# Performance work log

Measured on AMD Instinct MI355X. Metric: run time of the kernel, lower is better.

Reference implementation:

```python
import jax, jax.numpy as jnp
import numpy as np

T0, T1, LENGTH = 844, 1264, 8137


def setup_inputs() -> dict:
    key = jax.random.key(0)
    kq, = jax.random.split(key, 1)
    q = jax.random.normal(kq, (4, 8, LENGTH), dtype=jnp.float32)
    alpha0 = jnp.array(0.4886, dtype=jnp.float32)
    alpha1 = jnp.array(0.3893, dtype=jnp.float32)
    return {"q": q, "alpha0": alpha0, "alpha1": alpha1}


def reference(q, alpha0, alpha1):
    # A = I + alpha0 * superdiag(offset T0) + alpha1 * superdiag(offset T1)
    A = (jnp.eye(LENGTH, dtype=q.dtype)
         + alpha0 * jnp.eye(LENGTH, k=T0, dtype=q.dtype)
         + alpha1 * jnp.eye(LENGTH, k=T1, dtype=q.dtype))
    A_inv = jnp.linalg.inv(A)          # [L, L] dense inverse
    x = q @ A_inv                       # [B, C, L]
    loss = jnp.sum(x[0, 0, -T1:] ** 2)  # scalar
    return loss
```

## Files before the change

kernel.cpp:

```cpp
#include <hip/hip_runtime.h>


#define LENGTH 8137
#define T0 844
#define T1 1264

__global__ __launch_bounds__(256) void iir_loss_kernel(const float* __restrict__ q,
                                                       const float* __restrict__ alpha0,
                                                       const float* __restrict__ alpha1,
                                                       float* __restrict__ out) {
    __shared__ float x[LENGTH];
    __shared__ float partial[4];

    const float a0 = alpha0[0];
    const float a1 = alpha1[0];
    const int tid = threadIdx.x;

    const int nchunks = (LENGTH + T0 - 1) / T0;
    for (int c = 0; c < nchunks; ++c) {
        const int start = c * T0;
        const int end = (start + T0 < LENGTH) ? (start + T0) : LENGTH;
        for (int j = start + tid; j < end; j += 256) {
            float v = q[j];
            if (j >= T0) v -= a0 * x[j - T0];
            if (j >= T1) v -= a1 * x[j - T1];
            x[j] = v;
        }
        __syncthreads();
    }

    float s = 0.f;
    for (int j = (LENGTH - T1) + tid; j < LENGTH; j += 256) {
        s += x[j] * x[j];
    }
    for (int off = 32; off > 0; off >>= 1)
        s += __shfl_down(s, off, 64);
    const int wave = tid >> 6;
    if ((tid & 63) == 0) partial[wave] = s;
    __syncthreads();
    if (tid == 0) {
        float tot = partial[0] + partial[1] + partial[2] + partial[3];
        out[0] = tot;
    }
}

extern "C" void kernel_launch(void* const* d_in, const int* in_sizes, int n_in,
                              void* d_out, int out_size, void* d_ws, size_t ws_size,
                              hipStream_t stream) {
    const float* q      = (const float*)d_in[0];
    const float* alpha0 = (const float*)d_in[1];
    const float* alpha1 = (const float*)d_in[2];
    float* out = (float*)d_out;

    iir_loss_kernel<<<1, 256, 0, stream>>>(q, alpha0, alpha1, out);
}
```

Baseline: 68.20 us.

## Replace sequential IIR recurrence with closed-form binomial impulse-response expansion

Measured after the change: 59.81 us. -12.3%, faster.

```diff
diff --git a/kernel.cpp b/kernel.cpp
--- a/kernel.cpp
+++ b/kernel.cpp
@@ -4,44 +4,69 @@
 #define LENGTH 8137
 #define T0 844
 #define T1 1264
+#define JSTART (LENGTH - T1)
+#define MMAX 9
+#define NMAX 6
 
 __global__ __launch_bounds__(256) void iir_loss_kernel(const float* __restrict__ q,
-                                                       const float* __restrict__ alpha0,
-                                                       const float* __restrict__ alpha1,
+                                                       const float* __restrict__ a0p,
+                                                       const float* __restrict__ a1p,
                                                        float* __restrict__ out) {
-    __shared__ float x[LENGTH];
+    __shared__ float xq[LENGTH];
+    __shared__ float coef[NMAX + 1][MMAX + 1];
     __shared__ float partial[4];
 
-    const float a0 = alpha0[0];
-    const float a1 = alpha1[0];
     const int tid = threadIdx.x;
+    const float a0 = a0p[0];
+    const float a1 = a1p[0];
 
-    const int nchunks = (LENGTH + T0 - 1) / T0;
-    for (int c = 0; c < nchunks; ++c) {
-        const int start = c * T0;
-        const int end = (start + T0 < LENGTH) ? (start + T0) : LENGTH;
-        for (int j = start + tid; j < end; j += 256) {
-            float v = q[j];
-            if (j >= T0) v -= a0 * x[j - T0];
-            if (j >= T1) v -= a1 * x[j - T1];
-            x[j] = v;
+    const float4* q4 = reinterpret_cast<const float4*>(q);
+    for (int i = tid; i < LENGTH / 4; i += 256) {
+        float4 v = q4[i];
+        xq[4 * i + 0] = v.x;
+        xq[4 * i + 1] = v.y;
+        xq[4 * i + 2] = v.z;
+        xq[4 * i + 3] = v.w;
+    }
+    if (tid == 0) {
+        xq[LENGTH - 1] = q[LENGTH - 1];
+        coef[0][0] = 1.f;
+        for (int m = 1; m <= MMAX; ++m) coef[0][m] = -a0 * coef[0][m - 1];
+        for (int n = 1; n <= NMAX; ++n) {
+            coef[n][0] = -a1 * coef[n - 1][0];
+            for (int m = 1; m <= MMAX; ++m)
+                coef[n][m] = -a0 * coef[n][m - 1] - a1 * coef[n - 1][m];
         }
-        __syncthreads();
+    }
+    __syncthreads();
+
+    float v0 = 0.f, v1 = 0.f, v2 = 0.f, v3 = 0.f, v4 = 0.f;
+    const int j0 = JSTART + tid;
+    const bool has4 = (tid < (T1 - 4 * 256));
+
+    for (int n = 0; n <= NMAX; ++n) {
+        const int sn = T1 * n;
+        for (int m = 0; m <= MMAX; ++m) {
+            const int shift = sn + T0 * m;
+            if (shift >= LENGTH) break;
+            const float c = coef[n][m];
+            const int off = j0 - shift;
+            if (off >= 0)                 v0 += c * xq[off];
+            if (off + 256 >= 0)           v1 += c * xq[off + 256];
+            if (off + 512 >= 0)           v2 += c * xq[off + 512];
+            if (off + 768 >= 0)           v3 += c * xq[off + 768];
+            if (has4 && off + 1024 >= 0)  v4 += c * xq[off + 1024];
+        }
     }
 
-    float s = 0.f;
-    for (int j = (LENGTH - T1) + tid; j < LENGTH; j += 256) {
-        s += x[j] * x[j];
-    }
+    float s = v0 * v0 + v1 * v1 + v2 * v2 + v3 * v3 + v4 * v4;
+
     for (int off = 32; off > 0; off >>= 1)
         s += __shfl_down(s, off, 64);
-    const int wave = tid >> 6;
-    if ((tid & 63) == 0) partial[wave] = s;
+    if ((tid & 63) == 0) partial[tid >> 6] = s;
     __syncthreads();
-    if (tid == 0) {
-        float tot = partial[0] + partial[1] + partial[2] + partial[3];
-        out[0] = tot;
-    }
+    if (tid == 0)
+        out[0] = partial[0] + partial[1] + partial[2] + partial[3];
 }
 
 extern "C" void kernel_launch(void* const* d_in, const int* in_sizes, int n_in,
```
